# Performance work log

Hardware: AMD Instinct MI355X
Metric: run time of the kernel (lower is better)

## Reference

```python
import jax, jax.numpy as jnp
import numpy as np

B, N, KNN_K, T_FRAC = 8, 4096, 32, 0.5
C_IN, C_OUT = 4, 64


def _knn_group(q, db, kk):
    """q: [Nq,3] queries, db: [Nd,3] database. Returns feats [Nq,kk,4], nn [Nq,kk,3]."""
    d2 = (jnp.sum(q * q, axis=-1, keepdims=True)
          + jnp.sum(db * db, axis=-1)[None, :]
          - 2.0 * (q @ db.T))                      # [Nq,Nd] squared dists
    _, idx = jax.lax.top_k(-d2, kk)                 # ascending distance, like pytorch3d knn_points
    nn = db[idx]                                    # [Nq,kk,3]
    resi = nn - q[:, None, :]                       # [Nq,kk,3]
    sq = jnp.sum(resi * resi, axis=-1, keepdims=True)
    dist = jnp.where(sq > 0, jnp.sqrt(jnp.where(sq > 0, sq, 1.0)), 0.0)  # safe norm (exact fwd)
    feats = jnp.concatenate([resi, dist], axis=-1)  # [Nq,kk,4]
    return feats, nn


def _forward(points1, points2, pc, Wq, Wk, Wv, bq, bk, bv, ridx1, ridx2, k, t):
    k2 = int(k * t)
    k1 = k - k2
    p1 = jnp.swapaxes(points1, 1, 2)  # [B,N,3]
    p2 = jnp.swapaxes(points2, 1, 2)
    p3 = jnp.swapaxes(pc, 1, 2)

    def per_batch(a, b, c, i1, i2):
        newp = jnp.concatenate([a[i1], b[i2]], axis=0)     # [N,3] fused candidate set
        f1, g1 = _knn_group(newp, a, k1)
        f2, g2 = _knn_group(newp, b, k2)
        f3, g3 = _knn_group(newp, c, k)
        feats = jnp.concatenate([f1, f2, f3], axis=1)      # [N,2k,4]
        grouped = jnp.concatenate([g1, g2, g3], axis=1)    # [N,2k,3]
        return feats, grouped

    feats, grouped = jax.vmap(per_batch)(p1, p2, p3, ridx1, ridx2)  # [B,N,2k,4], [B,N,2k,3]

    # SelfAttention over the neighbor axis (per point group)
    q = feats @ Wq + bq          # [B,N,2k,C_OUT]
    kf = feats @ Wk + bk
    v = feats @ Wv + bv
    scale = 1.0 / np.sqrt(C_OUT).astype(np.float32)
    attn = jax.nn.softmax(jnp.einsum('bnkc,bnjc->bnkj', q, kf) * scale, axis=-1)
    y = jnp.einsum('bnkj,bnjc->bnkc', attn, v)             # [B,N,2k,C_OUT]

    score = jnp.max(y, axis=-1)                            # max over channels -> [B,N,2k]
    w = jax.nn.softmax(score, axis=-1)                     # weights over 2k neighbors
    fused = jnp.einsum('bnk,bnkd->bdn', w, grouped)        # [B,3,N]
    return fused


def setup_inputs() -> dict:
    key = jax.random.key(0)
    ks = jax.random.split(key, 8)
    points1 = jax.random.normal(ks[0], (B, 3, N), dtype=jnp.float32)
    points2 = jax.random.normal(ks[1], (B, 3, N), dtype=jnp.float32)
    pc = jax.random.normal(ks[2], (B, 3, N), dtype=jnp.float32)
    N2 = int(N * T_FRAC)
    N1 = N - N2
    perm = lambda kk: jax.random.permutation(kk, N)
    ridx1 = jax.vmap(perm)(jax.random.split(ks[3], B))[:, :N1].astype(jnp.int32)
    ridx2 = jax.vmap(perm)(jax.random.split(ks[4], B))[:, :N2].astype(jnp.int32)
    s = 1.0 / np.sqrt(C_IN)
    Wq = jax.random.normal(ks[5], (C_IN, C_OUT), dtype=jnp.float32) * s
    Wk = jax.random.normal(ks[6], (C_IN, C_OUT), dtype=jnp.float32) * s
    Wv = jax.random.normal(ks[7], (C_IN, C_OUT), dtype=jnp.float32) * s
    z = jnp.zeros((C_OUT,), dtype=jnp.float32)
    return {"points1": points1, "points2": points2, "pc": pc,
            "Wq": Wq, "Wk": Wk, "Wv": Wv, "bq": z, "bk": z, "bv": z,
            "ridx1": ridx1, "ridx2": ridx2, "k": KNN_K, "t": T_FRAC}


def reference(points1, points2, pc, Wq, Wk, Wv, bq, bk, bv, ridx1, ridx2, k, t):
    return _forward(points1, points2, pc, Wq, Wk, Wv, bq, bk, bv, ridx1, ridx2, k, t)
```

## Files before the change

### kernel.cpp

```cpp
#include <hip/hip_runtime.h>
#include <hip/hip_bf16.h>
#include <math.h>

#define NB   8
#define NPT  4096
#define NQ1  2048
#define NQ2  2048
#define KTOT 64
#define TILE 512
#define NTHR 256
#define QPB  128
#define TBUF 16

#define PRM_OFF (4u << 20)

__global__ void pf2_setup(const float* __restrict__ Wq, const float* __restrict__ Wk,
                          const float* __restrict__ bq, const float* __restrict__ bk,
                          float* __restrict__ prm) {
    int t = threadIdx.x;
    const float sc = 0.125f;
    if (t < 16) {
        int p = t >> 2, q = t & 3;
        float a = 0.f;
        for (int c = 0; c < 64; ++c) a += Wq[p * 64 + c] * Wk[q * 64 + c];
        prm[t] = a * sc;
    } else if (t < 20) {
        int p = t - 16; float a = 0.f;
        for (int c = 0; c < 64; ++c) a += Wq[p * 64 + c] * bk[c];
        prm[t] = a * sc;
    } else if (t < 24) {
        int q = t - 20; float a = 0.f;
        for (int c = 0; c < 64; ++c) a += Wk[q * 64 + c] * bq[c];
        prm[t] = a * sc;
    } else if (t == 24) {
        float a = 0.f;
        for (int c = 0; c < 64; ++c) a += bq[c] * bk[c];
        prm[t] = a * sc;
    }
}

template <int K>
__device__ __forceinline__ void insert_sorted(float (&dl)[K], int (&il)[K], float d, int id) {
#pragma unroll
    for (int j = 0; j < K; ++j) {
        bool sw = d < dl[j];
        float td = dl[j]; int ti = il[j];
        dl[j] = sw ? d : td;
        il[j] = sw ? id : ti;
        d  = sw ? td : d;
        id = sw ? ti : id;
    }
}

template <int K>
__device__ void knn_half(const float* __restrict__ dbp,
                         float qx, float qy, float qz, int tid,
                         float4* __restrict__ tileLds,
                         uint2* __restrict__ bufLds,
                         unsigned short* __restrict__ outIdx) {
    const int q = tid & (QPB - 1), h = tid >> 7;
    float dl[K]; int il[K];
#pragma unroll
    for (int j = 0; j < K; ++j) { dl[j] = INFINITY; il[j] = 0; }
    float thresh = INFINITY;
    int cnt = 0;
    float4* tp = tileLds + h * TILE;

    auto flush = [&]() {
        for (int u = 0; u < TBUF; ++u) {
            if (!__any(u < cnt)) break;
            if (u < cnt) {
                uint2 e = bufLds[u * NTHR + tid];
                float s = __uint_as_float(e.x);
                if (s < dl[K - 1]) insert_sorted<K>(dl, il, s, (int)e.y);
            }
        }
        cnt = 0;
        thresh = dl[K - 1];
    };

    for (int st = 0; st < 2048 / TILE; ++st) {
        int base = h * 2048 + st * TILE;
        __syncthreads();
        for (int r = 0; r < TILE / QPB; ++r) {
            int j = q + r * QPB;
            float x = dbp[base + j];
            float y = dbp[NPT + base + j];
            float z = dbp[2 * NPT + base + j];
            tp[j] = make_float4(-2.f * x, -2.f * y, -2.f * z,
                                fmaf(x, x, fmaf(y, y, z * z)));
        }
        __syncthreads();

        for (int c0 = 0; c0 < TILE; c0 += 8) {
            float sv[8];
#pragma unroll
            for (int u = 0; u < 8; ++u) {
                float4 p = tp[c0 + u];
                sv[u] = fmaf(p.x, qx, fmaf(p.y, qy, fmaf(p.z, qz, p.w)));
            }
#pragma unroll
            for (int u = 0; u < 8; ++u) {
                if (sv[u] < thresh) {
                    bufLds[cnt * NTHR + tid] =
                        make_uint2(__float_as_uint(sv[u]), (unsigned)(base + c0 + u));
                    ++cnt;
                }
            }
            if (__any(cnt > TBUF - 8)) flush();
        }
    }
    flush();

    float* mD = (float*)bufLds;
    unsigned short* mI = (unsigned short*)(mD + 32 * QPB);
    __syncthreads();
    if (h == 1) {
#pragma unroll
        for (int j = 0; j < K; ++j) {
            mD[j * QPB + q] = dl[j];
            mI[j * QPB + q] = (unsigned short)il[j];
        }
    }
    __syncthreads();
    if (h == 0) {
#pragma unroll
        for (int j = 0; j < K; ++j) {
            float d = mD[j * QPB + q];
            int id = (int)mI[j * QPB + q];
            if (d < dl[K - 1]) insert_sorted<K>(dl, il, d, id);
        }
        unsigned* o32 = (unsigned*)outIdx;
#pragma unroll
        for (int u = 0; u < K / 2; ++u)
            o32[u] = (unsigned)(unsigned short)il[2 * u] |
                     ((unsigned)(unsigned short)il[2 * u + 1] << 16);
    }
}

__global__ __launch_bounds__(NTHR) void pf2_knn(const float* __restrict__ p1,
                                                const float* __restrict__ p2,
                                                const float* __restrict__ pc,
                                                const int* __restrict__ ridx1,
                                                const int* __restrict__ ridx2,
                                                unsigned short* __restrict__ wsIdx) {
    __shared__ float4 tileLds[2 * TILE];
    __shared__ uint2  bufLds[TBUF * NTHR];

    int bid = blockIdx.x;
    int dbslot = bid >> 8;
    int db = (dbslot == 0) ? 2 : dbslot - 1;
    int rem = bid & 255;
    int b = rem >> 5;
    int chunk = rem & 31;
    int tid = threadIdx.x;
    int i = chunk * QPB + (tid & (QPB - 1));

    int j0; const float* srcp;
    if (i < NQ1) { j0 = ridx1[b * NQ1 + i]; srcp = p1; }
    else         { j0 = ridx2[b * NQ2 + (i - NQ1)]; srcp = p2; }
    const float* sb = srcp + (size_t)b * 3 * NPT;
    float qx = sb[j0], qy = sb[NPT + j0], qz = sb[2 * NPT + j0];

    const float* dbp = (db == 0 ? p1 : db == 1 ? p2 : pc) + (size_t)b * 3 * NPT;
    unsigned short* out = wsIdx + (size_t)(b * NPT + i) * KTOT +
                          (db == 0 ? 0 : db == 1 ? 16 : 32);
    if (db < 2) knn_half<16>(dbp, qx, qy, qz, tid, tileLds, bufLds, out);
    else        knn_half<32>(dbp, qx, qy, qz, tid, tileLds, bufLds, out);
}

__global__ __launch_bounds__(256) void pf2_attn(const float* __restrict__ p1,
                                                const float* __restrict__ p2,
                                                const float* __restrict__ pc,
                                                const int* __restrict__ ridx1,
                                                const int* __restrict__ ridx2,
                                                const float* __restrict__ Wv,
                                                const float* __restrict__ bv,
                                                const float* __restrict__ prm,
                                                const unsigned short* __restrict__ wsIdx,
                                                float* __restrict__ out) {
    __shared__ float4 wvt[64];
    __shared__ float  bvs[64];
    __shared__ float  prms[25];
    __shared__ float4 gl[4][64];
    __shared__ float4 fl[4][64];
    __shared__ float  sl[4][64];

    int tid = threadIdx.x;
    if (tid < 64) {
        wvt[tid] = make_float4(Wv[tid], Wv[64 + tid], Wv[128 + tid], Wv[192 + tid]);
        bvs[tid] = bv[tid];
    } else if (tid < 89) {
        prms[tid - 64] = prm[tid - 64];
    }
    __syncthreads();

    int wv = tid >> 6, lane = tid & 63;
    int g = blockIdx.x * 4 + wv;
    int b = g >> 12;
    int i = g & 4095;

    int j0; const float* srcp;
    if (i < NQ1) { j0 = ridx1[b * NQ1 + i]; srcp = p1; }
    else         { j0 = ridx2[b * NQ2 + (i - NQ1)]; srcp = p2; }
    const float* sb = srcp + (size_t)b * 3 * NPT;
    float qx = sb[j0], qy = sb[NPT + j0], qz = sb[2 * NPT + j0];

    int nidx = (int)wsIdx[(size_t)(b * NPT + i) * KTOT + lane];
    const float* dbp = (lane < 16 ? p1 : lane < 32 ? p2 : pc) + (size_t)b * 3 * NPT;
    float nx = dbp[nidx], ny = dbp[NPT + nidx], nz = dbp[2 * NPT + nidx];
    float fx = nx - qx, fy = ny - qy, fz = nz - qz;
    float sq = fx * fx + fy * fy + fz * fz;
    float fw = sq > 0.f ? sqrtf(sq) : 0.f;

    float gx = prms[0]  * fx + prms[1]  * fy + prms[2]  * fz + prms[3]  * fw;
    float gy = prms[4]  * fx + prms[5]  * fy + prms[6]  * fz + prms[7]  * fw;
    float gz = prms[8]  * fx + prms[9]  * fy + prms[10] * fz + prms[11] * fw;
    float gw = prms[12] * fx + prms[13] * fy + prms[14] * fz + prms[15] * fw;
    float sj = prms[20] * fx + prms[21] * fy + prms[22] * fz + prms[23] * fw;

    gl[wv][lane] = make_float4(gx, gy, gz, gw);
    fl[wv][lane] = make_float4(fx, fy, fz, fw);
    sl[wv][lane] = sj;
    __syncthreads();

    float m = -INFINITY;
    for (int j = 0; j < 64; ++j) {
        float4 gj = gl[wv][j];
        float l = fx * gj.x + fy * gj.y + fz * gj.z + fw * gj.w + sl[wv][j];
        m = fmaxf(m, l);
    }
    float S = 0.f, H0 = 0.f, H1 = 0.f, H2 = 0.f, H3 = 0.f;
    for (int j = 0; j < 64; ++j) {
        float4 gj = gl[wv][j];
        float4 fj = fl[wv][j];
        float l = fx * gj.x + fy * gj.y + fz * gj.z + fw * gj.w + sl[wv][j];
        float e = __expf(l - m);
        S += e;
        H0 += e * fj.x; H1 += e * fj.y; H2 += e * fj.z; H3 += e * fj.w;
    }
    float rS = 1.f / S;

    float smax = -INFINITY;
    for (int ch = 0; ch < 64; ++ch) {
        float4 wc = wvt[ch];
        float t = H0 * wc.x + H1 * wc.y + H2 * wc.z + H3 * wc.w;
        float yv = fmaf(t, rS, bvs[ch]);
        smax = fmaxf(smax, yv);
    }

    float M = smax;
    for (int off = 32; off; off >>= 1) M = fmaxf(M, __shfl_xor(M, off));
    float e = __expf(smax - M);
    float E = e;
    for (int off = 32; off; off >>= 1) E += __shfl_xor(E, off);
    float w = e / E;
    float px = w * nx, py = w * ny, pz = w * nz;
    for (int off = 32; off; off >>= 1) {
        px += __shfl_xor(px, off);
        py += __shfl_xor(py, off);
        pz += __shfl_xor(pz, off);
    }
    if (lane == 0) {
        float* ob = out + (size_t)b * 3 * NPT + i;
        ob[0] = px; ob[NPT] = py; ob[2 * NPT] = pz;
    }
}

extern "C" void kernel_launch(void* const* d_in, const int* in_sizes, int n_in,
                              void* d_out, int out_size, void* d_ws, size_t ws_size,
                              hipStream_t stream) {
    const float* p1 = (const float*)d_in[0];
    const float* p2 = (const float*)d_in[1];
    const float* pc = (const float*)d_in[2];
    const float* Wq = (const float*)d_in[3];
    const float* Wk = (const float*)d_in[4];
    const float* Wv = (const float*)d_in[5];
    const float* bq = (const float*)d_in[6];
    const float* bk = (const float*)d_in[7];
    const float* bv = (const float*)d_in[8];
    const int* ridx1 = (const int*)d_in[9];
    const int* ridx2 = (const int*)d_in[10];
    float* out = (float*)d_out;

    unsigned short* wsIdx = (unsigned short*)d_ws;
    float* prm = (float*)((char*)d_ws + PRM_OFF);

    pf2_setup<<<1, 32, 0, stream>>>(Wq, Wk, bq, bk, prm);
    pf2_knn<<<NB * 3 * (NPT / QPB), NTHR, 0, stream>>>(p1, p2, pc, ridx1, ridx2, wsIdx);
    pf2_attn<<<NB * NPT / 4, 256, 0, stream>>>(p1, p2, pc, ridx1, ridx2, Wv, bv, prm, wsIdx, out);
}
```

Measured before the change: 399.0 us.

## Scan full database per thread instead of splitting halves across two threads

```diff
diff --git a/kernel.cpp b/kernel.cpp
--- a/kernel.cpp
+++ b/kernel.cpp
@@ -7,10 +7,9 @@
 #define NQ1  2048
 #define NQ2  2048
 #define KTOT 64
-#define TILE 512
-#define NTHR 256
-#define QPB  128
-#define TBUF 16
+#define TILE 1024
+#define NTHR 128
+#define TBUF 24
 
 #define PRM_OFF (4u << 20)
 
@@ -53,42 +52,41 @@
 }
 
 template <int K>
-__device__ void knn_half(const float* __restrict__ dbp,
+__device__ void knn_full(const float* __restrict__ dbp,
                          float qx, float qy, float qz, int tid,
                          float4* __restrict__ tileLds,
                          uint2* __restrict__ bufLds,
                          unsigned short* __restrict__ outIdx) {
-    const int q = tid & (QPB - 1), h = tid >> 7;
     float dl[K]; int il[K];
 #pragma unroll
     for (int j = 0; j < K; ++j) { dl[j] = INFINITY; il[j] = 0; }
     float thresh = INFINITY;
     int cnt = 0;
-    float4* tp = tileLds + h * TILE;
 
     auto flush = [&]() {
         for (int u = 0; u < TBUF; ++u) {
             if (!__any(u < cnt)) break;
-            if (u < cnt) {
-                uint2 e = bufLds[u * NTHR + tid];
-                float s = __uint_as_float(e.x);
-                if (s < dl[K - 1]) insert_sorted<K>(dl, il, s, (int)e.y);
+            uint2 e = bufLds[u * NTHR + tid];
+            float s = __uint_as_float(e.x);
+            bool pass = (u < cnt) && (s < dl[K - 1]);
+            if (__any(pass)) {
+                if (pass) insert_sorted<K>(dl, il, s, (int)e.y);
             }
         }
         cnt = 0;
         thresh = dl[K - 1];
     };
 
-    for (int st = 0; st < 2048 / TILE; ++st) {
-        int base = h * 2048 + st * TILE;
+    for (int st = 0; st < NPT / TILE; ++st) {
+        int base = st * TILE;
         __syncthreads();
-        for (int r = 0; r < TILE / QPB; ++r) {
-            int j = q + r * QPB;
+        for (int r = 0; r < TILE / NTHR; ++r) {
+            int j = tid + r * NTHR;
             float x = dbp[base + j];
             float y = dbp[NPT + base + j];
             float z = dbp[2 * NPT + base + j];
-            tp[j] = make_float4(-2.f * x, -2.f * y, -2.f * z,
-                                fmaf(x, x, fmaf(y, y, z * z)));
+            tileLds[j] = make_float4(-2.f * x, -2.f * y, -2.f * z,
+                                     fmaf(x, x, fmaf(y, y, z * z)));
         }
         __syncthreads();
 
@@ -96,7 +94,7 @@
             float sv[8];
 #pragma unroll
             for (int u = 0; u < 8; ++u) {
-                float4 p = tp[c0 + u];
+                float4 p = tileLds[c0 + u];
                 sv[u] = fmaf(p.x, qx, fmaf(p.y, qy, fmaf(p.z, qz, p.w)));
             }
 #pragma unroll
@@ -112,30 +110,11 @@
     }
     flush();
 
-    float* mD = (float*)bufLds;
-    unsigned short* mI = (unsigned short*)(mD + 32 * QPB);
-    __syncthreads();
-    if (h == 1) {
-#pragma unroll
-        for (int j = 0; j < K; ++j) {
-            mD[j * QPB + q] = dl[j];
-            mI[j * QPB + q] = (unsigned short)il[j];
-        }
-    }
-    __syncthreads();
-    if (h == 0) {
-#pragma unroll
-        for (int j = 0; j < K; ++j) {
-            float d = mD[j * QPB + q];
-            int id = (int)mI[j * QPB + q];
-            if (d < dl[K - 1]) insert_sorted<K>(dl, il, d, id);
-        }
-        unsigned* o32 = (unsigned*)outIdx;
-#pragma unroll
-        for (int u = 0; u < K / 2; ++u)
-            o32[u] = (unsigned)(unsigned short)il[2 * u] |
-                     ((unsigned)(unsigned short)il[2 * u + 1] << 16);
-    }
+    unsigned* o32 = (unsigned*)outIdx;
+#pragma unroll
+    for (int u = 0; u < K / 2; ++u)
+        o32[u] = (unsigned)(unsigned short)il[2 * u] |
+                 ((unsigned)(unsigned short)il[2 * u + 1] << 16);
 }
 
 __global__ __launch_bounds__(NTHR) void pf2_knn(const float* __restrict__ p1,
@@ -144,7 +123,7 @@
                                                 const int* __restrict__ ridx1,
                                                 const int* __restrict__ ridx2,
                                                 unsigned short* __restrict__ wsIdx) {
-    __shared__ float4 tileLds[2 * TILE];
+    __shared__ float4 tileLds[TILE];
     __shared__ uint2  bufLds[TBUF * NTHR];
 
     int bid = blockIdx.x;
@@ -154,7 +133,7 @@
     int b = rem >> 5;
     int chunk = rem & 31;
     int tid = threadIdx.x;
-    int i = chunk * QPB + (tid & (QPB - 1));
+    int i = chunk * NTHR + tid;
 
     int j0; const float* srcp;
     if (i < NQ1) { j0 = ridx1[b * NQ1 + i]; srcp = p1; }
@@ -165,8 +144,8 @@
     const float* dbp = (db == 0 ? p1 : db == 1 ? p2 : pc) + (size_t)b * 3 * NPT;
     unsigned short* out = wsIdx + (size_t)(b * NPT + i) * KTOT +
                           (db == 0 ? 0 : db == 1 ? 16 : 32);
-    if (db < 2) knn_half<16>(dbp, qx, qy, qz, tid, tileLds, bufLds, out);
-    else        knn_half<32>(dbp, qx, qy, qz, tid, tileLds, bufLds, out);
+    if (db < 2) knn_full<16>(dbp, qx, qy, qz, tid, tileLds, bufLds, out);
+    else        knn_full<32>(dbp, qx, qy, qz, tid, tileLds, bufLds, out);
 }
 
 __global__ __launch_bounds__(256) void pf2_attn(const float* __restrict__ p1,
@@ -287,6 +266,6 @@
     float* prm = (float*)((char*)d_ws + PRM_OFF);
 
     pf2_setup<<<1, 32, 0, stream>>>(Wq, Wk, bq, bk, prm);
-    pf2_knn<<<NB * 3 * (NPT / QPB), NTHR, 0, stream>>>(p1, p2, pc, ridx1, ridx2, wsIdx);
+    pf2_knn<<<NB * 3 * (NPT / NTHR), NTHR, 0, stream>>>(p1, p2, pc, ridx1, ridx2, wsIdx);
     pf2_attn<<<NB * NPT / 4, 256, 0, stream>>>(p1, p2, pc, ridx1, ridx2, Wv, bv, prm, wsIdx, out);
 }
```

Measured after the change: 538.3 us. +34.9%, slower.
